# Performance work log

Hardware: AMD Instinct MI355X
Metric: run time of the kernel (lower is better)

Reference implementation:

```python
import jax, jax.numpy as jnp
import numpy as np

EPS = 1e-5  # torch LayerNorm default
DT_RANK = 32  # ceil(d_model=512 / 16)


def layer_norm(x, g, b):
    mu = x.mean(-1, keepdims=True)
    var = x.var(-1, keepdims=True)
    return (x - mu) / jnp.sqrt(var + EPS) * g + b


def conv1d(x, w, b, pad):
    # x: (B, C, L), w: (O, I, K) -- torch Conv1d semantics
    y = jax.lax.conv_general_dilated(x, w, (1,), [(pad, pad)],
                                     dimension_numbers=('NCH', 'OIH', 'NCH'))
    return y + b[None, :, None]


def mamba(u, in_w, conv_w, conv_b, xproj_w, dt_w, dt_b, Alog, D, out_w, d_state, d_conv):
    # Faithful mamba_ssm Mamba block (no biases on in/x/out proj, RMS of official impl)
    Bsz, L, _ = u.shape
    xz = jnp.einsum('bld,ed->ble', u, in_w)          # (B, L, 2*Di)
    x, z = jnp.split(xz, 2, axis=-1)
    Di = x.shape[-1]
    # causal depthwise conv1d, truncated to L (padding=d_conv-1 on the left)
    xc = jax.lax.conv_general_dilated(x.transpose(0, 2, 1), conv_w[:, None, :], (1,),
                                      [(d_conv - 1, 0)],
                                      dimension_numbers=('NCH', 'OIH', 'NCH'),
                                      feature_group_count=Di)
    x = jax.nn.silu((xc + conv_b[None, :, None]).transpose(0, 2, 1))  # (B, L, Di)
    xdb = jnp.einsum('bld,ed->ble', x, xproj_w)       # (B, L, dt_rank + 2*N)
    dt = jax.nn.softplus(jnp.einsum('blr,dr->bld', xdb[..., :DT_RANK], dt_w) + dt_b)
    Bm = xdb[..., DT_RANK:DT_RANK + d_state]          # (B, L, N)
    Cm = xdb[..., DT_RANK + d_state:]                 # (B, L, N)
    A = -jnp.exp(Alog)                                # (Di, N)

    def step(h, ins):
        dt_t, x_t, B_t, C_t = ins                     # (B,Di),(B,Di),(B,N),(B,N)
        dA = jnp.exp(dt_t[..., None] * A)             # (B, Di, N)
        h = dA * h + (dt_t * x_t)[..., None] * B_t[:, None, :]
        y = (h * C_t[:, None, :]).sum(-1)             # (B, Di)
        return h, y

    h0 = jnp.zeros((Bsz, Di, d_state), u.dtype)
    xs = (dt.transpose(1, 0, 2), x.transpose(1, 0, 2),
          Bm.transpose(1, 0, 2), Cm.transpose(1, 0, 2))
    _, ys = jax.lax.scan(step, h0, xs)
    y = ys.transpose(1, 0, 2) + x * D                 # skip via D
    y = y * jax.nn.silu(z)
    return jnp.einsum('bld,od->blo', y, out_w)


def _forward(x, fe_w, fe_b, fe_ln_g, fe_ln_b, emb_ln_g, emb_ln_b,
             conv1_w, conv1_b, conv2_w, conv2_b,
             mf_in_w, mf_conv_w, mf_conv_b, mf_xproj_w, mf_dt_w, mf_dt_b, mf_Alog, mf_D, mf_out_w,
             mb_in_w, mb_conv_w, mb_conv_b, mb_xproj_w, mb_dt_w, mb_dt_b, mb_Alog, mb_D, mb_out_w,
             norm_g, norm_b, fc1_w, fc1_b, fc2_w, fc2_b):
    x = x.reshape(x.shape[0], 100, 23)
    # FrequencyEmbedding: rfft over a length-1 last dim == the signal itself; |.| then Linear+LN+ReLU
    id_mag = jnp.abs(x[..., :1])                      # (B, 100, 1)
    e = jax.nn.relu(layer_norm(id_mag @ fe_w.T + fe_b, fe_ln_g, fe_ln_b))
    id_embed = jax.nn.relu(layer_norm(e, emb_ln_g, emb_ln_b))  # outer LN+ReLU
    data = x[..., 1:].transpose(0, 2, 1)              # (B, 22, 100)
    f1 = jax.nn.relu(conv1d(data, conv1_w, conv1_b, 1))
    f2 = jax.nn.relu(conv1d(f1, conv2_w, conv2_b, 1)).transpose(0, 2, 1)  # (B,100,256)
    comb = jnp.concatenate([id_embed, f2], axis=-1)   # (B, 100, 512)
    fo = mamba(comb, mf_in_w, mf_conv_w, mf_conv_b, mf_xproj_w, mf_dt_w, mf_dt_b,
               mf_Alog, mf_D, mf_out_w, 16, 4)
    bo = mamba(comb[:, ::-1], mb_in_w, mb_conv_w, mb_conv_b, mb_xproj_w, mb_dt_w, mb_dt_b,
               mb_Alog, mb_D, mb_out_w, 8, 2)[:, ::-1]
    pooled = (fo + bo).max(axis=1)                    # (B, 512)
    pooled = layer_norm(pooled, norm_g, norm_b)       # self.norm (undefined in source; LN(512))
    h = jax.nn.relu(pooled @ fc1_w.T + fc1_b)
    return h @ fc2_w.T + fc2_b                        # (B, 4)


def setup_inputs() -> dict:
    key = jax.random.key(0)
    ks = iter(jax.random.split(key, 48))
    def n(shape, s=0.02):
        return jax.random.normal(next(ks), shape, jnp.float32) * s
    Di = 1024
    alog16 = jnp.log(jnp.tile(jnp.arange(1, 17, dtype=jnp.float32), (Di, 1)))
    alog8 = jnp.log(jnp.tile(jnp.arange(1, 9, dtype=jnp.float32), (Di, 1)))
    return {
        'x': jax.random.normal(next(ks), (512, 2300), jnp.float32),
        'fe_w': n((256, 1), 1.0), 'fe_b': jnp.zeros(256, jnp.float32),
        'fe_ln_g': jnp.ones(256, jnp.float32), 'fe_ln_b': jnp.zeros(256, jnp.float32),
        'emb_ln_g': jnp.ones(256, jnp.float32), 'emb_ln_b': jnp.zeros(256, jnp.float32),
        'conv1_w': n((128, 22, 3)), 'conv1_b': jnp.zeros(128, jnp.float32),
        'conv2_w': n((256, 128, 3)), 'conv2_b': jnp.zeros(256, jnp.float32),
        'mf_in_w': n((2 * Di, 512)), 'mf_conv_w': n((Di, 4)), 'mf_conv_b': jnp.zeros(Di, jnp.float32),
        'mf_xproj_w': n((32 + 2 * 16, Di)), 'mf_dt_w': n((Di, 32)), 'mf_dt_b': n((Di,), 0.1),
        'mf_Alog': alog16, 'mf_D': jnp.ones(Di, jnp.float32), 'mf_out_w': n((512, Di)),
        'mb_in_w': n((2 * Di, 512)), 'mb_conv_w': n((Di, 2)), 'mb_conv_b': jnp.zeros(Di, jnp.float32),
        'mb_xproj_w': n((32 + 2 * 8, Di)), 'mb_dt_w': n((Di, 32)), 'mb_dt_b': n((Di,), 0.1),
        'mb_Alog': alog8, 'mb_D': jnp.ones(Di, jnp.float32), 'mb_out_w': n((512, Di)),
        'norm_g': jnp.ones(512, jnp.float32), 'norm_b': jnp.zeros(512, jnp.float32),
        'fc1_w': n((128, 512)), 'fc1_b': jnp.zeros(128, jnp.float32),
        'fc2_w': n((4, 128)), 'fc2_b': jnp.zeros(4, jnp.float32),
    }


def reference(x, fe_w, fe_b, fe_ln_g, fe_ln_b, emb_ln_g, emb_ln_b,
              conv1_w, conv1_b, conv2_w, conv2_b,
              mf_in_w, mf_conv_w, mf_conv_b, mf_xproj_w, mf_dt_w, mf_dt_b, mf_Alog, mf_D, mf_out_w,
              mb_in_w, mb_conv_w, mb_conv_b, mb_xproj_w, mb_dt_w, mb_dt_b, mb_Alog, mb_D, mb_out_w,
              norm_g, norm_b, fc1_w, fc1_b, fc2_w, fc2_b):
    return _forward(x, fe_w, fe_b, fe_ln_g, fe_ln_b, emb_ln_g, emb_ln_b,
                    conv1_w, conv1_b, conv2_w, conv2_b,
                    mf_in_w, mf_conv_w, mf_conv_b, mf_xproj_w, mf_dt_w, mf_dt_b, mf_Alog, mf_D, mf_out_w,
                    mb_in_w, mb_conv_w, mb_conv_b, mb_xproj_w, mb_dt_w, mb_dt_b, mb_Alog, mb_D, mb_out_w,
                    norm_g, norm_b, fc1_w, fc1_b, fc2_w, fc2_b)
```

## Files before the change

### kernel.cpp

```cpp
#include <hip/hip_runtime.h>
#include <cstddef>
#include <cstdint>

#define BSZ 512
#define SEQ 100

typedef __bf16 bf16_t;
typedef __attribute__((ext_vector_type(8))) __bf16 bf16x8;
typedef __attribute__((ext_vector_type(4))) float f32x4;

__device__ __forceinline__ float sigmoidf_(float v){ return 1.f/(1.f + __expf(-v)); }
__device__ __forceinline__ float siluf_(float v){ return v * sigmoidf_(v); }
__device__ __forceinline__ float softplusf_(float v){ return (v > 20.f) ? v : __logf(1.f + __expf(v)); }

__global__ __launch_bounds__(256) void cvt_bf16_kernel(
    const float* __restrict__ src, bf16_t* __restrict__ dst, int n)
{
    int i = blockIdx.x*256 + threadIdx.x;
    if (i < n) dst[i] = (bf16_t)src[i];
}

__global__ __launch_bounds__(256) void prep_outw_kernel(
    const float* __restrict__ of, const float* __restrict__ ob, bf16_t* __restrict__ W)
{
    int i = blockIdx.x*256 + threadIdx.x;
    if (i < 512*2048){
        int o = i >> 11, k = i & 2047;
        W[i] = (bf16_t)((k < 1024) ? of[o*1024 + k] : ob[o*1024 + (k - 1024)]);
    }
}

__global__ __launch_bounds__(256) void prep_convw_kernel(
    const float* __restrict__ c1w, const float* __restrict__ c2w,
    bf16_t* __restrict__ W1p, bf16_t* __restrict__ W2p)
{
    int i = blockIdx.x*256 + threadIdx.x;
    if (i < 128*96){
        int o = i / 96, kk = i - o*96, k = kk >> 5, c = kk & 31;
        W1p[i] = (c < 22) ? (bf16_t)c1w[(o*22 + c)*3 + k] : (bf16_t)0.f;
    }
    if (i < 256*384){
        int o = i / 384, kk = i - o*384, k = kk >> 7, c = kk & 127;
        W2p[i] = (bf16_t)c2w[(o*128 + c)*3 + k];
    }
}

__global__ __launch_bounds__(256) void fe0_kernel(
    const float* __restrict__ x,
    const float* __restrict__ fe_w, const float* __restrict__ fe_b,
    const float* __restrict__ g1, const float* __restrict__ b1,
    const float* __restrict__ g2, const float* __restrict__ b2,
    bf16_t* __restrict__ comb, bf16_t* __restrict__ F0pad, bf16_t* __restrict__ F1pad)
{
    const int b = blockIdx.x;
    const int t = threadIdx.x;
    const int wv = t >> 6, lane = t & 63;

    float few[4], feb[4], lg1[4], lb1[4], lg2[4], lb2[4];
    #pragma unroll
    for (int q = 0; q < 4; ++q){
        int j = lane + 64*q;
        few[q] = fe_w[j]; feb[q] = fe_b[j];
        lg1[q] = g1[j];  lb1[q] = b1[j];
        lg2[q] = g2[j];  lb2[q] = b2[j];
    }
    for (int l = wv; l < SEQ; l += 4){
        float m = fabsf(x[(size_t)(b*SEQ + l)*23]);
        float e[4];
        float s1 = 0.f, s2 = 0.f;
        #pragma unroll
        for (int q = 0; q < 4; ++q){ e[q] = m*few[q] + feb[q]; s1 += e[q]; s2 += e[q]*e[q]; }
        #pragma unroll
        for (int off = 32; off > 0; off >>= 1){ s1 += __shfl_xor(s1, off); s2 += __shfl_xor(s2, off); }
        float mean = s1 * (1.f/256.f);
        float rstd = rsqrtf(s2*(1.f/256.f) - mean*mean + 1e-5f);
        s1 = 0.f; s2 = 0.f;
        #pragma unroll
        for (int q = 0; q < 4; ++q){
            e[q] = fmaxf((e[q]-mean)*rstd*lg1[q] + lb1[q], 0.f);
            s1 += e[q]; s2 += e[q]*e[q];
        }
        #pragma unroll
        for (int off = 32; off > 0; off >>= 1){ s1 += __shfl_xor(s1, off); s2 += __shfl_xor(s2, off); }
        mean = s1 * (1.f/256.f);
        rstd = rsqrtf(s2*(1.f/256.f) - mean*mean + 1e-5f);
        #pragma unroll
        for (int q = 0; q < 4; ++q){
            float v = fmaxf((e[q]-mean)*rstd*lg2[q] + lb2[q], 0.f);
            comb[(size_t)(b*SEQ + l)*512 + lane + 64*q] = (bf16_t)v;
        }
    }

    for (int idx = t; idx < 102*32; idx += 256){
        int r = idx >> 5, c = idx & 31;
        float v = 0.f;
        if (r >= 1 && r <= SEQ && c < 22) v = x[(size_t)(b*SEQ + r - 1)*23 + 1 + c];
        F0pad[(size_t)(b*102 + r)*32 + c] = (bf16_t)v;
    }
    if (t < 128) F1pad[(size_t)(b*102 + 0)*128 + t] = (bf16_t)0.f;
    else F1pad[(size_t)(b*102 + 101)*128 + (t - 128)] = (bf16_t)0.f;
}

__global__ __launch_bounds__(256) void gemm_conv_kernel(
    const bf16_t* __restrict__ Abase, int lda, int Az,
    const bf16_t* __restrict__ W, int K, int N,
    const float* __restrict__ bias,
    bf16_t* __restrict__ Cbase, int ldc, int Cb, int coff, int noff, int Mtot)
{
    __shared__ bf16_t As[128*32];
    __shared__ bf16_t Ws[128*32];
    const bf16_t* A = Abase + (size_t)blockIdx.z * Az;
    const int t = threadIdx.x;
    const int lane = t & 63, w = t >> 6;
    const int n0 = blockIdx.y * 128;
    const int rsub = lane >> 2, csub = lane & 3;
    const int col = lane & 15, quad = lane >> 4;
    const int wOffM = (w & 1) * 64, wOffN = (w >> 1) * 64;

    f32x4 acc[4][4];
    #pragma unroll
    for (int i = 0; i < 4; ++i)
        #pragma unroll
        for (int j = 0; j < 4; ++j)
            acc[i][j] = (f32x4){0.f, 0.f, 0.f, 0.f};

    for (int k0 = 0; k0 < K; k0 += 32){
        __syncthreads();
        #pragma unroll
        for (int q = 0; q < 2; ++q){
            const int rt = w*32 + q*16 + rsub;
            const int lq = csub ^ ((rt >> 1) & 3);
            int ra = (rt < Mtot) ? rt : (Mtot - 1);
            const bf16_t* ga = A + (size_t)ra*lda + k0 + lq*8;
            __builtin_amdgcn_global_load_lds(
                (const __attribute__((address_space(1))) void*)ga,
                (__attribute__((address_space(3))) void*)&As[(w*32 + q*16)*32], 16, 0, 0);
            const bf16_t* gw = W + (size_t)(n0 + rt)*K + k0 + lq*8;
            __builtin_amdgcn_global_load_lds(
                (const __attribute__((address_space(1))) void*)gw,
                (__attribute__((address_space(3))) void*)&Ws[(w*32 + q*16)*32], 16, 0, 0);
        }
        __syncthreads();

        bf16x8 af[4], bfv[4];
        #pragma unroll
        for (int i = 0; i < 4; ++i){
            const int ra = wOffM + i*16 + col;
            af[i]  = *(const bf16x8*)&As[ra*32 + (quad ^ ((ra >> 1) & 3))*8];
            const int rb = wOffN + i*16 + col;
            bfv[i] = *(const bf16x8*)&Ws[rb*32 + (quad ^ ((rb >> 1) & 3))*8];
        }
        #pragma unroll
        for (int i = 0; i < 4; ++i)
            #pragma unroll
            for (int j = 0; j < 4; ++j)
                acc[i][j] = __builtin_amdgcn_mfma_f32_16x16x32_bf16(af[i], bfv[j], acc[i][j], 0, 0, 0);
    }

    #pragma unroll
    for (int i = 0; i < 4; ++i){
        const int gmb = wOffM + i*16 + quad*4;
        #pragma unroll
        for (int j = 0; j < 4; ++j){
            const int gn = n0 + wOffN + j*16 + col;
            const float bb = bias[gn];
            #pragma unroll
            for (int r = 0; r < 4; ++r){
                const int gm = gmb + r;
                if (gm < Mtot){
                    float v = fmaxf(acc[i][j][r] + bb, 0.f);
                    Cbase[((size_t)blockIdx.z*Cb + coff + gm)*ldc + noff + gn] = (bf16_t)v;
                }
            }
        }
    }
}

__global__ __launch_bounds__(256) void gemm_in_kernel(
    const bf16_t* __restrict__ A, int lda, int Mtot,
    const bf16_t* __restrict__ W, int K,
    bf16_t* __restrict__ xy, bf16_t* __restrict__ z)
{
    __shared__ bf16_t smem[128*132];
    bf16_t* As0 = smem;
    bf16_t* As1 = smem + 4096;
    bf16_t* Ws0 = smem + 8192;
    bf16_t* Ws1 = smem + 12288;
    const int t = threadIdx.x;
    const int lane = t & 63, w = t >> 6;
    const int m0 = blockIdx.x * 128, n0 = blockIdx.y * 128;
    const int rsub = lane >> 2, csub = lane & 3;
    const int col = lane & 15, quad = lane >> 4;
    const int wOffM = (w & 1) * 64, wOffN = (w >> 1) * 64;

    f32x4 acc[4][4];
    #pragma unroll
    for (int i = 0; i < 4; ++i)
        #pragma unroll
        for (int j = 0; j < 4; ++j)
            acc[i][j] = (f32x4){0.f, 0.f, 0.f, 0.f};

    for (int k0 = 0; k0 < K; k0 += 64){
        __syncthreads();
        #pragma unroll
        for (int hh = 0; hh < 2; ++hh){
            bf16_t* Asb = hh ? As1 : As0;
            bf16_t* Wsb = hh ? Ws1 : Ws0;
            #pragma unroll
            for (int q = 0; q < 2; ++q){
                const int rt = w*32 + q*16 + rsub;
                const int lq = csub ^ ((rt >> 1) & 3);
                int ra = m0 + rt; ra = (ra < Mtot) ? ra : (Mtot - 1);
                const bf16_t* ga = A + (size_t)ra*lda + k0 + hh*32 + lq*8;
                __builtin_amdgcn_global_load_lds(
                    (const __attribute__((address_space(1))) void*)ga,
                    (__attribute__((address_space(3))) void*)&Asb[(w*32 + q*16)*32], 16, 0, 0);
                const bf16_t* gw = W + (size_t)(n0 + rt)*K + k0 + hh*32 + lq*8;
                __builtin_amdgcn_global_load_lds(
                    (const __attribute__((address_space(1))) void*)gw,
                    (__attribute__((address_space(3))) void*)&Wsb[(w*32 + q*16)*32], 16, 0, 0);
            }
        }
        __syncthreads();

        #pragma unroll
        for (int hh = 0; hh < 2; ++hh){
            bf16_t* Asb = hh ? As1 : As0;
            bf16_t* Wsb = hh ? Ws1 : Ws0;
            bf16x8 af[4], bfv[4];
            #pragma unroll
            for (int i = 0; i < 4; ++i){
                const int ra = wOffM + i*16 + col;
                af[i]  = *(const bf16x8*)&Asb[ra*32 + (quad ^ ((ra >> 1) & 3))*8];
                const int rb = wOffN + i*16 + col;
                bfv[i] = *(const bf16x8*)&Wsb[rb*32 + (quad ^ ((rb >> 1) & 3))*8];
            }
            #pragma unroll
            for (int i = 0; i < 4; ++i)
                #pragma unroll
                for (int j = 0; j < 4; ++j)
                    acc[i][j] = __builtin_amdgcn_mfma_f32_16x16x32_bf16(af[i], bfv[j], acc[i][j], 0, 0, 0);
        }
    }

    __syncthreads();
    #pragma unroll
    for (int i = 0; i < 4; ++i){
        const int row0 = wOffM + i*16 + quad*4;
        #pragma unroll
        for (int j = 0; j < 4; ++j){
            const int cT = wOffN + j*16 + col;
            #pragma unroll
            for (int r = 0; r < 4; ++r)
                smem[(row0 + r)*132 + cT] = (bf16_t)acc[i][j][r];
        }
    }
    __syncthreads();

    const int half = n0 >> 11, within = n0 & 2047;
    bf16_t* dstBase = ((within < 1024) ? xy : z) + half*1024 + (within & 1023);
    #pragma unroll
    for (int k = 0; k < 8; ++k){
        const int idx = t + k*256;
        const int row = idx >> 4;
        const int ch  = (idx & 15) * 8;
        const int gm = m0 + row;
        if (gm < Mtot)
            *(bf16x8*)&dstBase[(size_t)gm*2048 + ch] = *(const bf16x8*)&smem[row*132 + ch];
    }
}

__global__ __launch_bounds__(256) void gemm_out_kernel(
    const bf16_t* __restrict__ A, int Mtot,
    const bf16_t* __restrict__ W,
    float* __restrict__ C)
{
    __shared__ bf16_t As[2][128*32];
    __shared__ bf16_t Ws[2][128*32];
    const int t = threadIdx.x;
    const int lane = t & 63, w = t >> 6;
    const int m0 = blockIdx.x * 128, n0 = blockIdx.y * 128;
    const int rsub = lane >> 2, csub = lane & 3;
    const int col = lane & 15, quad = lane >> 4;
    const int wOffM = (w & 1) * 64, wOffN = (w >> 1) * 64;
    const int K = 2048;

    f32x4 acc[4][4];
    #pragma unroll
    for (int i = 0; i < 4; ++i)
        #pragma unroll
        for (int j = 0; j < 4; ++j)
            acc[i][j] = (f32x4){0.f, 0.f, 0.f, 0.f};

    for (int k0 = 0; k0 < K; k0 += 64){
        __syncthreads();
        #pragma unroll
        for (int hh = 0; hh < 2; ++hh){
            #pragma unroll
            for (int q = 0; q < 2; ++q){
                const int rt = w*32 + q*16 + rsub;
                const int lq = csub ^ ((rt >> 1) & 3);
                int ra = m0 + rt; ra = (ra < Mtot) ? ra : (Mtot - 1);
                const bf16_t* ga = A + (size_t)ra*K + k0 + hh*32 + lq*8;
                __builtin_amdgcn_global_load_lds(
                    (const __attribute__((address_space(1))) void*)ga,
                    (__attribute__((address_space(3))) void*)&As[hh][(w*32 + q*16)*32], 16, 0, 0);
                const bf16_t* gw = W + (size_t)(n0 + rt)*K + k0 + hh*32 + lq*8;
                __builtin_amdgcn_global_load_lds(
                    (const __attribute__((address_space(1))) void*)gw,
                    (__attribute__((address_space(3))) void*)&Ws[hh][(w*32 + q*16)*32], 16, 0, 0);
            }
        }
        __syncthreads();

        #pragma unroll
        for (int hh = 0; hh < 2; ++hh){
            bf16x8 af[4], bfv[4];
            #pragma unroll
            for (int i = 0; i < 4; ++i){
                const int ra = wOffM + i*16 + col;
                af[i]  = *(const bf16x8*)&As[hh][ra*32 + (quad ^ ((ra >> 1) & 3))*8];
                const int rb = wOffN + i*16 + col;
                bfv[i] = *(const bf16x8*)&Ws[hh][rb*32 + (quad ^ ((rb >> 1) & 3))*8];
            }
            #pragma unroll
            for (int i = 0; i < 4; ++i)
                #pragma unroll
                for (int j = 0; j < 4; ++j)
                    acc[i][j] = __builtin_amdgcn_mfma_f32_16x16x32_bf16(af[i], bfv[j], acc[i][j], 0, 0, 0);
        }
    }

    #pragma unroll
    for (int i = 0; i < 4; ++i){
        const int gmb = m0 + wOffM + i*16 + quad*4;
        #pragma unroll
        for (int j = 0; j < 4; ++j){
            const int gn = n0 + wOffN + j*16 + col;
            #pragma unroll
            for (int r = 0; r < 4; ++r){
                const int gm = gmb + r;
                if (gm < Mtot)
                    C[(size_t)gm*512 + gn] = acc[i][j][r];
            }
        }
    }
}

__global__ __launch_bounds__(256) void gemm_x_kernel(
    const bf16_t* __restrict__ xy,
    const bf16_t* __restrict__ Wf, const bf16_t* __restrict__ Wb,
    float* __restrict__ C)
{
    __shared__ bf16_t As[128*32];
    __shared__ bf16_t Ws[64*32];
    const int half = blockIdx.y;
    const bf16_t* A = xy + half*1024;
    const bf16_t* W = half ? Wb : Wf;
    const int N = half ? 48 : 64;
    const int t = threadIdx.x;
    const int lane = t & 63, w = t >> 6;
    const int m0 = blockIdx.x * 128;
    const int rsub = lane >> 2, csub = lane & 3;
    const int col = lane & 15, quad = lane >> 4;

    f32x4 acc[2][4];
    #pragma unroll
    for (int i = 0; i < 2; ++i)
        #pragma unroll
        for (int j = 0; j < 4; ++j)
            acc[i][j] = (f32x4){0.f, 0.f, 0.f, 0.f};

    for (int k0 = 0; k0 < 1024; k0 += 32){
        __syncthreads();
        #pragma unroll
        for (int q = 0; q < 2; ++q){
            const int rt = q*64 + w*16 + rsub;
            const int lq = csub ^ ((rt >> 1) & 3);
            const bf16_t* ga = A + (size_t)(m0 + rt)*2048 + k0 + lq*8;
            __builtin_amdgcn_global_load_lds(
                (const __attribute__((address_space(1))) void*)ga,
                (__attribute__((address_space(3))) void*)&As[(q*64 + w*16)*32], 16, 0, 0);
        }
        {
            const int rt = w*16 + rsub;
            const int lq = csub ^ ((rt >> 1) & 3);
            int rw = (rt < N) ? rt : (N - 1);
            const bf16_t* gw = W + (size_t)rw*1024 + k0 + lq*8;
            __builtin_amdgcn_global_load_lds(
                (const __attribute__((address_space(1))) void*)gw,
                (__attribute__((address_space(3))) void*)&Ws[(w*16)*32], 16, 0, 0);
        }
        __syncthreads();

        bf16x8 af[2], bfv[4];
        #pragma unroll
        for (int i = 0; i < 2; ++i){
            const int ra = w*32 + i*16 + col;
            af[i]  = *(const bf16x8*)&As[ra*32 + (quad ^ ((ra >> 1) & 3))*8];
        }
        #pragma unroll
        for (int j = 0; j < 4; ++j){
            const int rb = j*16 + col;
            bfv[j] = *(const bf16x8*)&Ws[rb*32 + (quad ^ ((rb >> 1) & 3))*8];
        }
        #pragma unroll
        for (int i = 0; i < 2; ++i)
            #pragma unroll
            for (int j = 0; j < 4; ++j)
                acc[i][j] = __builtin_amdgcn_mfma_f32_16x16x32_bf16(af[i], bfv[j], acc[i][j], 0, 0, 0);
    }

    #pragma unroll
    for (int i = 0; i < 2; ++i){
        const int gmb = m0 + w*32 + i*16 + quad*4;
        #pragma unroll
        for (int j = 0; j < 4; ++j){
            const int gn = j*16 + col;
            if (gn < N){
                #pragma unroll
                for (int r = 0; r < 4; ++r)
                    C[(size_t)(gmb + r)*128 + half*64 + gn] = acc[i][j][r];
            }
        }
    }
}

__global__ __launch_bounds__(256) void dt_kernel(
    const float* __restrict__ xdb,
    const float* __restrict__ dtwf, const float* __restrict__ dtbf,
    const float* __restrict__ dtwb, const float* __restrict__ dtbb,
    bf16_t* __restrict__ dtb)
{
    const int half = blockIdx.y >> 3;
    const int d = (blockIdx.y & 7)*128 + (threadIdx.x & 127);
    const int mslot = threadIdx.x >> 7;
    const int m0 = blockIdx.x * 16;
    __shared__ float sd[16*32];
    for (int i = threadIdx.x; i < 16*32; i += 256){
        int r = i >> 5, c = i & 31;
        sd[i] = xdb[(size_t)(m0 + r)*128 + half*64 + c];
    }
    const float* dw = half ? dtwb : dtwf;
    float w[32];
    #pragma unroll
    for (int r = 0; r < 32; ++r) w[r] = dw[d*32 + r];
    const float db = half ? dtbb[d] : dtbf[d];
    __syncthreads();
    #pragma unroll
    for (int i = 0; i < 8; ++i){
        const int row = mslot + i*2;
        const float* rp = &sd[row*32];
        float a = db;
        #pragma unroll
        for (int r = 0; r < 32; ++r) a += w[r]*rp[r];
        dtb[(size_t)(m0 + row)*2048 + half*1024 + d] = (bf16_t)softplusf_(a);
    }
}

template<int DC, bool REV>
__device__ __forceinline__ void conv_dev(bf16_t* base, const float* wsrc, float bias)
{
    float w[DC];
    #pragma unroll
    for (int k = 0; k < DC; ++k) w[k] = wsrc[k];
    float hist[DC-1];
    #pragma unroll
    for (int k = 0; k < DC-1; ++k) hist[k] = 0.f;
    const int step = REV ? -1 : 1;
    int l = REV ? (SEQ-1) : 0;
    for (int t0 = 0; t0 < SEQ; t0 += 10){
        float v[10];
        #pragma unroll
        for (int i = 0; i < 10; ++i) v[i] = (float)base[(size_t)(l + step*i)*2048];
        float o[10];
        #pragma unroll
        for (int i = 0; i < 10; ++i){
            float a = bias + w[DC-1]*v[i];
            #pragma unroll
            for (int j = 1; j < DC; ++j) a += w[DC-1-j]*hist[j-1];
            #pragma unroll
            for (int j = DC-2; j >= 1; --j) hist[j] = hist[j-1];
            hist[0] = v[i];
            o[i] = siluf_(a);
        }
        #pragma unroll
        for (int i = 0; i < 10; ++i)
            base[(size_t)(l + step*i)*2048] = (bf16_t)o[i];
        l += step*10;
    }
}

__global__ __launch_bounds__(256) void conv_silu_kernel(
    bf16_t* __restrict__ xy,
    const float* __restrict__ cwf, const float* __restrict__ cbf,
    const float* __restrict__ cwb, const float* __restrict__ cbb)
{
    const int gid = blockIdx.x*256 + threadIdx.x;
    const int b = gid >> 11, d2 = gid & 2047;
    const int half = d2 >> 10, d = d2 & 1023;
    bf16_t* base = xy + (size_t)b*SEQ*2048 + d2;
    if (half == 0) conv_dev<4, false>(base, cwf + d*4, cbf[d]);
    else           conv_dev<2, true >(base, cwb + d*2, cbb[d]);
}

template<int DS, bool REV, bool STRUCT>
__device__ __forceinline__ void scan_core(
    bf16_t* __restrict__ xybase, const bf16_t* __restrict__ zbase,
    const bf16_t* __restrict__ tbase, const float* __restrict__ sx,
    const float* __restrict__ Av, float Dd)
{
    float h[DS];
    #pragma unroll
    for (int s = 0; s < DS; ++s) h[s] = 0.f;
    const int step = REV ? -1 : 1;
    const float A0 = Av[0];
    int l = REV ? (SEQ-1) : 0;

    for (int t0 = 0; t0 < SEQ; t0 += 10){
        float xr[10], zr[10], tr[10];
        #pragma unroll
        for (int i = 0; i < 10; ++i){
            const size_t li = (size_t)(l + step*i);
            xr[i] = (float)xybase[li*2048];
            zr[i] = (float)zbase[li*2048];
            tr[i] = (float)tbase[li*2048];
        }
        #pragma unroll
        for (int i = 0; i < 10; ++i){
            const int li = l + step*i;
            const float4* sxl4 = (const float4*)&sx[li*2*DS];
            const float dtv = tr[i];
            const float dtx = dtv * xr[i];
            float yv = 0.f;
            if (STRUCT){
                const float r = __expf(dtv*A0);
                float rp = r;
                #pragma unroll
                for (int s4 = 0; s4 < DS/4; ++s4){
                    float4 Bv = sxl4[s4];
                    float4 Cv = sxl4[DS/4 + s4];
                    h[s4*4+0] = rp*h[s4*4+0] + dtx*Bv.x; yv += h[s4*4+0]*Cv.x; rp *= r;
                    h[s4*4+1] = rp*h[s4*4+1] + dtx*Bv.y; yv += h[s4*4+1]*Cv.y; rp *= r;
                    h[s4*4+2] = rp*h[s4*4+2] + dtx*Bv.z; yv += h[s4*4+2]*Cv.z; rp *= r;
                    h[s4*4+3] = rp*h[s4*4+3] + dtx*Bv.w; yv += h[s4*4+3]*Cv.w; rp *= r;
                }
            } else {
                #pragma unroll
                for (int s4 = 0; s4 < DS/4; ++s4){
                    float4 Bv = sxl4[s4];
                    float4 Cv = sxl4[DS/4 + s4];
                    h[s4*4+0] = __expf(dtv*Av[s4*4+0])*h[s4*4+0] + dtx*Bv.x; yv += h[s4*4+0]*Cv.x;
                    h[s4*4+1] = __expf(dtv*Av[s4*4+1])*h[s4*4+1] + dtx*Bv.y; yv += h[s4*4+1]*Cv.y;
                    h[s4*4+2] = __expf(dtv*Av[s4*4+2])*h[s4*4+2] + dtx*Bv.z; yv += h[s4*4+2]*Cv.z;
                    h[s4*4+3] = __expf(dtv*Av[s4*4+3])*h[s4*4+3] + dtx*Bv.w; yv += h[s4*4+3]*Cv.w;
                }
            }
            yv += xr[i]*Dd;
            yv *= siluf_(zr[i]);
            xybase[(size_t)li*2048] = (bf16_t)yv;
        }
        l += step*10;
    }
}

template<int DS, bool REV>
__device__ __forceinline__ void scan_dev(
    bf16_t* __restrict__ xybase, const bf16_t* __restrict__ zbase,
    const bf16_t* __restrict__ tbase, const float* __restrict__ sx,
    const float* __restrict__ Arow, float Dd)
{
    float Av[DS];
    #pragma unroll
    for (int s = 0; s < DS; ++s) Av[s] = -__expf(Arow[s]);
    bool structured = true;
    #pragma unroll
    for (int s = 1; s < DS; ++s)
        structured = structured && (fabsf(Av[s] - (float)(s+1)*Av[0]) <= 1e-4f*(float)(s+1));
    if (structured) scan_core<DS, REV, true >(xybase, zbase, tbase, sx, Av, Dd);
    else            scan_core<DS, REV, false>(xybase, zbase, tbase, sx, Av, Dd);
}

__global__ __launch_bounds__(256) void scan_kernel(
    bf16_t* __restrict__ xy, const bf16_t* __restrict__ z,
    const bf16_t* __restrict__ dtb, const float* __restrict__ xdb,
    const float* __restrict__ Alogf, const float* __restrict__ Dpf,
    const float* __restrict__ Alogb, const float* __restrict__ Dpb)
{
    const int b = blockIdx.x >> 3, s8 = blockIdx.x & 7;
    const int t = threadIdx.x;
    __shared__ float sxF[SEQ*32];
    __shared__ float sxB[SEQ*16];
    const float4* src = (const float4*)(xdb + (size_t)b*SEQ*128);

    {
        float4* dstF = (float4*)sxF;
        for (int i = t; i < SEQ*8; i += 256){
            int row = i >> 3, c = i & 7;
            dstF[row*8 + c] = src[row*32 + 8 + c];
        }
        float4* dstB = (float4*)sxB;
        for (int i = t; i < SEQ*4; i += 256){
            int row = i >> 2, c = i & 3;
            dstB[row*4 + c] = src[row*32 + 24 + c];
        }
    }
    __syncthreads();

    if (t < 128){
        const int d = s8*128 + t;
        const size_t off = (size_t)b*SEQ*2048 + d;
        scan_dev<16, false>(xy + off, z + off, dtb + off, sxF, Alogf + d*16, Dpf[d]);
    } else {
        const int d = s8*128 + (t - 128);
        const size_t off = (size_t)b*SEQ*2048 + 1024 + d;
        scan_dev<8, true>(xy + off, z + off, dtb + off, sxB, Alogb + d*8, Dpb[d]);
    }
}

__global__ __launch_bounds__(256) void head_kernel(
    const float* __restrict__ acc,
    const float* __restrict__ ng, const float* __restrict__ nb,
    const float* __restrict__ w1, const float* __restrict__ b1,
    const float* __restrict__ w2, const float* __restrict__ b2,
    float* __restrict__ out)
{
    const int b = blockIdx.x, t = threadIdx.x;
    __shared__ float4 sm4[256];
    __shared__ float sp[512];
    __shared__ float sh2[256];
    __shared__ float sh[128];
    __shared__ float red1[4], red2[4];
    const float* base = acc + (size_t)b*SEQ*512;

    {
        const int c4 = t & 127, lh = t >> 7;
        float4 m = make_float4(-3.4e38f, -3.4e38f, -3.4e38f, -3.4e38f);
        for (int l = lh*50; l < lh*50 + 50; ++l){
            float4 v = ((const float4*)(base + (size_t)l*512))[c4];
            m.x = fmaxf(m.x, v.x); m.y = fmaxf(m.y, v.y);
            m.z = fmaxf(m.z, v.z); m.w = fmaxf(m.w, v.w);
        }
        sm4[t] = m;
    }
    __syncthreads();
    if (t < 128){
        float4 a = sm4[t], c = sm4[t + 128];
        ((float4*)sp)[t] = make_float4(fmaxf(a.x,c.x), fmaxf(a.y,c.y),
                                       fmaxf(a.z,c.z), fmaxf(a.w,c.w));
    }
    __syncthreads();

    float s1 = 0.f, s2 = 0.f;
    for (int o = t; o < 512; o += 256){ float v = sp[o]; s1 += v; s2 += v*v; }
    #pragma unroll
    for (int off = 32; off > 0; off >>= 1){ s1 += __shfl_xor(s1, off); s2 += __shfl_xor(s2, off); }
    const int wv = t >> 6, lane = t & 63;
    if (lane == 0){ red1[wv] = s1; red2[wv] = s2; }
    __syncthreads();
    if (t == 0){
        float a = 0.f, c = 0.f;
        for (int i = 0; i < 4; ++i){ a += red1[i]; c += red2[i]; }
        float mean = a * (1.f/512.f);
        float var = c * (1.f/512.f) - mean*mean;
        red1[0] = mean; red2[0] = rsqrtf(var + 1e-5f);
    }
    __syncthreads();
    const float mean = red1[0], rstd = red2[0];
    for (int o = t; o < 512; o += 256) sp[o] = (sp[o]-mean)*rstd*ng[o] + nb[o];
    __syncthreads();

    {
        const int o = t & 127, half = t >> 7;
        const float4* wrow = (const float4*)(w1 + (size_t)o*512 + half*256);
        const float4* sp4 = (const float4*)sp + half*64;
        float s = 0.f;
        #pragma unroll 8
        for (int j = 0; j < 64; ++j){
            float4 a = sp4[j], wq = wrow[j];
            s += a.x*wq.x + a.y*wq.y + a.z*wq.z + a.w*wq.w;
        }
        sh2[t] = s;
    }
    __syncthreads();
    if (t < 128) sh[t] = fmaxf(sh2[t] + sh2[t + 128] + b1[t], 0.f);
    __syncthreads();
    if (t < 4){
        float a = b2[t];
        for (int j = 0; j < 128; ++j) a += sh[j]*w2[t*128 + j];
        out[b*4 + t] = a;
    }
}

extern "C" void kernel_launch(void* const* d_in, const int* in_sizes, int n_in,
                              void* d_out, int out_size, void* d_ws, size_t ws_size,
                              hipStream_t stream)
{
    (void)in_sizes; (void)n_in; (void)out_size;
    const float* x        = (const float*)d_in[0];
    const float* fe_w     = (const float*)d_in[1];
    const float* fe_b     = (const float*)d_in[2];
    const float* fe_ln_g  = (const float*)d_in[3];
    const float* fe_ln_b  = (const float*)d_in[4];
    const float* emb_ln_g = (const float*)d_in[5];
    const float* emb_ln_b = (const float*)d_in[6];
    const float* conv1_w  = (const float*)d_in[7];
    const float* conv1_b  = (const float*)d_in[8];
    const float* conv2_w  = (const float*)d_in[9];
    const float* conv2_b  = (const float*)d_in[10];
    const float* mf_in_w  = (const float*)d_in[11];
    const float* mf_conv_w= (const float*)d_in[12];
    const float* mf_conv_b= (const float*)d_in[13];
    const float* mf_xproj = (const float*)d_in[14];
    const float* mf_dt_w  = (const float*)d_in[15];
    const float* mf_dt_b  = (const float*)d_in[16];
    const float* mf_Alog  = (const float*)d_in[17];
    const float* mf_D     = (const float*)d_in[18];
    const float* mf_out_w = (const float*)d_in[19];
    const float* mb_in_w  = (const float*)d_in[20];
    const float* mb_conv_w= (const float*)d_in[21];
    const float* mb_conv_b= (const float*)d_in[22];
    const float* mb_xproj = (const float*)d_in[23];
    const float* mb_dt_w  = (const float*)d_in[24];
    const float* mb_dt_b  = (const float*)d_in[25];
    const float* mb_Alog  = (const float*)d_in[26];
    const float* mb_D     = (const float*)d_in[27];
    const float* mb_out_w = (const float*)d_in[28];
    const float* norm_g   = (const float*)d_in[29];
    const float* norm_b   = (const float*)d_in[30];
    const float* fc1_w    = (const float*)d_in[31];
    const float* fc1_b    = (const float*)d_in[32];
    const float* fc2_w    = (const float*)d_in[33];
    const float* fc2_b    = (const float*)d_in[34];
    float* out = (float*)d_out;

    char* p = (char*)d_ws;
    bf16_t* w_in   = (bf16_t*)p; p += (size_t)4096*512*sizeof(bf16_t);
    bf16_t* w_out  = (bf16_t*)p; p += (size_t)512*2048*sizeof(bf16_t);
    bf16_t* w_xpf  = (bf16_t*)p; p += (size_t)64*1024*sizeof(bf16_t);
    bf16_t* w_xpb  = (bf16_t*)p; p += (size_t)48*1024*sizeof(bf16_t);
    bf16_t* W1p    = (bf16_t*)p; p += (size_t)128*96*sizeof(bf16_t);
    bf16_t* W2p    = (bf16_t*)p; p += (size_t)256*384*sizeof(bf16_t);
    bf16_t* comb_all = (bf16_t*)p; p += (size_t)BSZ*SEQ*512*sizeof(bf16_t);
    const size_t fixed_bytes = (size_t)(p - (char*)d_ws);

    const size_t per_b = (size_t)SEQ * (2048*2 + 2048*2 + 2048*2 + 128*4);
    const size_t budget = (ws_size > fixed_bytes) ? (ws_size - fixed_bytes) : 0;
    int Bc = BSZ;
    while (Bc > 64 && (size_t)Bc * per_b > budget) Bc >>= 1;
    const int nch = BSZ / Bc;
    const int M = Bc * SEQ;

    bf16_t* F0pad = (bf16_t*)p;
    bf16_t* F1pad = F0pad + (size_t)BSZ*102*32;
    bf16_t* xy   = (bf16_t*)p;               p += (size_t)M*2048*sizeof(bf16_t);
    bf16_t* z    = (bf16_t*)p;               p += (size_t)M*2048*sizeof(bf16_t);
    bf16_t* dtb  = (bf16_t*)p;               p += (size_t)M*2048*sizeof(bf16_t);
    float*  xdb  = (float*)p;
    float*  accb = (float*)dtb;

    cvt_bf16_kernel<<<(2048*512+255)/256, 256, 0, stream>>>(mf_in_w, w_in, 2048*512);
    cvt_bf16_kernel<<<(2048*512+255)/256, 256, 0, stream>>>(mb_in_w, w_in + (size_t)2048*512, 2048*512);
    prep_outw_kernel<<<(512*2048+255)/256, 256, 0, stream>>>(mf_out_w, mb_out_w, w_out);
    cvt_bf16_kernel<<<(64*1024+255)/256,  256, 0, stream>>>(mf_xproj, w_xpf, 64*1024);
    cvt_bf16_kernel<<<(48*1024+255)/256,  256, 0, stream>>>(mb_xproj, w_xpb, 48*1024);
    prep_convw_kernel<<<(256*384+255)/256, 256, 0, stream>>>(conv1_w, conv2_w, W1p, W2p);

    fe0_kernel<<<BSZ, 256, 0, stream>>>(x, fe_w, fe_b, fe_ln_g, fe_ln_b,
        emb_ln_g, emb_ln_b, comb_all, F0pad, F1pad);
    gemm_conv_kernel<<<dim3(1, 1, BSZ), 256, 0, stream>>>(
        F0pad, 32, 102*32, W1p, 96, 128, conv1_b, F1pad, 128, 102, 1, 0, SEQ);
    gemm_conv_kernel<<<dim3(1, 2, BSZ), 256, 0, stream>>>(
        F1pad, 128, 102*128, W2p, 384, 256, conv2_b, comb_all, 512, 100, 0, 256, SEQ);

    const int gm128 = M / 128;

    for (int c = 0; c < nch; ++c){
        const size_t b0 = (size_t)c * Bc;
        const bf16_t* comb = comb_all + b0*SEQ*512;

        gemm_in_kernel<<<dim3(gm128, 32), 256, 0, stream>>>(comb, 512, M, w_in, 512, xy, z);
        conv_silu_kernel<<<Bc*2048/256, 256, 0, stream>>>(xy, mf_conv_w, mf_conv_b,
                                                          mb_conv_w, mb_conv_b);
        gemm_x_kernel<<<dim3(gm128, 2), 256, 0, stream>>>(xy, w_xpf, w_xpb, xdb);
        dt_kernel<<<dim3(M/16, 16), 256, 0, stream>>>(xdb, mf_dt_w, mf_dt_b,
                                                      mb_dt_w, mb_dt_b, dtb);
        scan_kernel<<<Bc*8, 256, 0, stream>>>(xy, z, dtb, xdb,
                                              mf_Alog, mf_D, mb_Alog, mb_D);
        gemm_out_kernel<<<dim3(gm128, 4), 256, 0, stream>>>(xy, M, w_out, accb);
        head_kernel<<<Bc, 256, 0, stream>>>(accb, norm_g, norm_b, fc1_w, fc1_b,
                                            fc2_w, fc2_b, out + b0*4);
    }
}
```

Before: 1.529 ms.

## Fuse dt projection and softplus into x-projection GEMM epilogue using MFMA

```diff
diff --git a/kernel.cpp b/kernel.cpp
--- a/kernel.cpp
+++ b/kernel.cpp
@@ -350,13 +350,18 @@
 __global__ __launch_bounds__(256) void gemm_x_kernel(
     const bf16_t* __restrict__ xy,
     const bf16_t* __restrict__ Wf, const bf16_t* __restrict__ Wb,
-    float* __restrict__ C)
+    const bf16_t* __restrict__ dWf, const bf16_t* __restrict__ dWb,
+    const float* __restrict__ dbf, const float* __restrict__ dbb,
+    float* __restrict__ C,
+    bf16_t* __restrict__ dtb)
 {
     __shared__ bf16_t As[128*32];
-    __shared__ bf16_t Ws[64*32];
+    __shared__ bf16_t Ws[128*32];
     const int half = blockIdx.y;
     const bf16_t* A = xy + half*1024;
     const bf16_t* W = half ? Wb : Wf;
+    const bf16_t* dW = half ? dWb : dWf;
+    const float* db = half ? dbb : dbf;
     const int N = half ? 48 : 64;
     const int t = threadIdx.x;
     const int lane = t & 63, w = t >> 6;
@@ -424,37 +429,66 @@
             }
         }
     }
-}
-
-__global__ __launch_bounds__(256) void dt_kernel(
-    const float* __restrict__ xdb,
-    const float* __restrict__ dtwf, const float* __restrict__ dtbf,
-    const float* __restrict__ dtwb, const float* __restrict__ dtbb,
-    bf16_t* __restrict__ dtb)
-{
-    const int half = blockIdx.y >> 3;
-    const int d = (blockIdx.y & 7)*128 + (threadIdx.x & 127);
-    const int mslot = threadIdx.x >> 7;
-    const int m0 = blockIdx.x * 16;
-    __shared__ float sd[16*32];
-    for (int i = threadIdx.x; i < 16*32; i += 256){
-        int r = i >> 5, c = i & 31;
-        sd[i] = xdb[(size_t)(m0 + r)*128 + half*64 + c];
-    }
-    const float* dw = half ? dtwb : dtwf;
-    float w[32];
-    #pragma unroll
-    for (int r = 0; r < 32; ++r) w[r] = dw[d*32 + r];
-    const float db = half ? dtbb[d] : dtbf[d];
-    __syncthreads();
-    #pragma unroll
-    for (int i = 0; i < 8; ++i){
-        const int row = mslot + i*2;
-        const float* rp = &sd[row*32];
-        float a = db;
-        #pragma unroll
-        for (int r = 0; r < 32; ++r) a += w[r]*rp[r];
-        dtb[(size_t)(m0 + row)*2048 + half*1024 + d] = (bf16_t)softplusf_(a);
+
+    __syncthreads();
+    #pragma unroll
+    for (int i = 0; i < 2; ++i){
+        const int row0 = w*32 + i*16 + quad*4;
+        #pragma unroll
+        for (int j = 0; j < 2; ++j){
+            const int cc = j*16 + col;
+            #pragma unroll
+            for (int r = 0; r < 4; ++r){
+                const int row = row0 + r;
+                const int pc = (cc >> 3) ^ ((row >> 1) & 3);
+                As[row*32 + pc*8 + (cc & 7)] = (bf16_t)acc[i][j][r];
+            }
+        }
+    }
+
+    const int wOffM = (w & 1)*64, wOffN = (w >> 1)*64;
+    for (int n2 = 0; n2 < 8; ++n2){
+        __syncthreads();
+        #pragma unroll
+        for (int q = 0; q < 2; ++q){
+            const int rt = w*32 + q*16 + rsub;
+            const int lq = csub ^ ((rt >> 1) & 3);
+            const bf16_t* gw = dW + (size_t)(n2*128 + rt)*32 + lq*8;
+            __builtin_amdgcn_global_load_lds(
+                (const __attribute__((address_space(1))) void*)gw,
+                (__attribute__((address_space(3))) void*)&Ws[(w*32 + q*16)*32], 16, 0, 0);
+        }
+        __syncthreads();
+
+        bf16x8 af[4], bfv[4];
+        #pragma unroll
+        for (int i = 0; i < 4; ++i){
+            const int ra = wOffM + i*16 + col;
+            af[i]  = *(const bf16x8*)&As[ra*32 + (quad ^ ((ra >> 1) & 3))*8];
+            const int rb = wOffN + i*16 + col;
+            bfv[i] = *(const bf16x8*)&Ws[rb*32 + (quad ^ ((rb >> 1) & 3))*8];
+        }
+        f32x4 a2[4][4];
+        #pragma unroll
+        for (int i = 0; i < 4; ++i)
+            #pragma unroll
+            for (int j = 0; j < 4; ++j)
+                a2[i][j] = __builtin_amdgcn_mfma_f32_16x16x32_bf16(
+                    af[i], bfv[j], (f32x4){0.f,0.f,0.f,0.f}, 0, 0, 0);
+
+        #pragma unroll
+        for (int i = 0; i < 4; ++i){
+            const int gmb = m0 + wOffM + i*16 + quad*4;
+            #pragma unroll
+            for (int j = 0; j < 4; ++j){
+                const int gn = n2*128 + wOffN + j*16 + col;
+                const float bb = db[gn];
+                #pragma unroll
+                for (int r = 0; r < 4; ++r)
+                    dtb[(size_t)(gmb + r)*2048 + half*1024 + gn] =
+                        (bf16_t)softplusf_(a2[i][j][r] + bb);
+            }
+        }
     }
 }
 
@@ -472,7 +506,7 @@
     for (int t0 = 0; t0 < SEQ; t0 += 10){
         float v[10];
         #pragma unroll
-        for (int i = 0; i < 10; ++i) v[i] = (float)base[(size_t)(l + step*i)*2048];
+        for (int i = 0; i < 10; ++i) v[i] = (float)base[(l + step*i)*2048];
         float o[10];
         #pragma unroll
         for (int i = 0; i < 10; ++i){
@@ -486,7 +520,7 @@
         }
         #pragma unroll
         for (int i = 0; i < 10; ++i)
-            base[(size_t)(l + step*i)*2048] = (bf16_t)o[i];
+            base[(l + step*i)*2048] = (bf16_t)o[i];
         l += step*10;
     }
 }
@@ -521,10 +555,10 @@
         float xr[10], zr[10], tr[10];
         #pragma unroll
         for (int i = 0; i < 10; ++i){
-            const size_t li = (size_t)(l + step*i);
-            xr[i] = (float)xybase[li*2048];
-            zr[i] = (float)zbase[li*2048];
-            tr[i] = (float)tbase[li*2048];
+            const int li = (l + step*i)*2048;
+            xr[i] = (float)xybase[li];
+            zr[i] = (float)zbase[li];
+            tr[i] = (float)tbase[li];
         }
         #pragma unroll
         for (int i = 0; i < 10; ++i){
@@ -558,7 +592,7 @@
             }
             yv += xr[i]*Dd;
             yv *= siluf_(zr[i]);
-            xybase[(size_t)li*2048] = (bf16_t)yv;
+            xybase[li*2048] = (bf16_t)yv;
         }
         l += step*10;
     }
@@ -739,6 +773,8 @@
     bf16_t* w_out  = (bf16_t*)p; p += (size_t)512*2048*sizeof(bf16_t);
     bf16_t* w_xpf  = (bf16_t*)p; p += (size_t)64*1024*sizeof(bf16_t);
     bf16_t* w_xpb  = (bf16_t*)p; p += (size_t)48*1024*sizeof(bf16_t);
+    bf16_t* w_dtf  = (bf16_t*)p; p += (size_t)1024*32*sizeof(bf16_t);
+    bf16_t* w_dtb  = (bf16_t*)p; p += (size_t)1024*32*sizeof(bf16_t);
     bf16_t* W1p    = (bf16_t*)p; p += (size_t)128*96*sizeof(bf16_t);
     bf16_t* W2p    = (bf16_t*)p; p += (size_t)256*384*sizeof(bf16_t);
     bf16_t* comb_all = (bf16_t*)p; p += (size_t)BSZ*SEQ*512*sizeof(bf16_t);
@@ -764,6 +800,8 @@
     prep_outw_kernel<<<(512*2048+255)/256, 256, 0, stream>>>(mf_out_w, mb_out_w, w_out);
     cvt_bf16_kernel<<<(64*1024+255)/256,  256, 0, stream>>>(mf_xproj, w_xpf, 64*1024);
     cvt_bf16_kernel<<<(48*1024+255)/256,  256, 0, stream>>>(mb_xproj, w_xpb, 48*1024);
+    cvt_bf16_kernel<<<(1024*32+255)/256,  256, 0, stream>>>(mf_dt_w, w_dtf, 1024*32);
+    cvt_bf16_kernel<<<(1024*32+255)/256,  256, 0, stream>>>(mb_dt_w, w_dtb, 1024*32);
     prep_convw_kernel<<<(256*384+255)/256, 256, 0, stream>>>(conv1_w, conv2_w, W1p, W2p);
 
     fe0_kernel<<<BSZ, 256, 0, stream>>>(x, fe_w, fe_b, fe_ln_g, fe_ln_b,
@@ -782,9 +820,9 @@
         gemm_in_kernel<<<dim3(gm128, 32), 256, 0, stream>>>(comb, 512, M, w_in, 512, xy, z);
         conv_silu_kernel<<<Bc*2048/256, 256, 0, stream>>>(xy, mf_conv_w, mf_conv_b,
                                                           mb_conv_w, mb_conv_b);
-        gemm_x_kernel<<<dim3(gm128, 2), 256, 0, stream>>>(xy, w_xpf, w_xpb, xdb);
-        dt_kernel<<<dim3(M/16, 16), 256, 0, stream>>>(xdb, mf_dt_w, mf_dt_b,
-                                                      mb_dt_w, mb_dt_b, dtb);
+        gemm_x_kernel<<<dim3(gm128, 2), 256, 0, stream>>>(xy, w_xpf, w_xpb,
+                                                          w_dtf, w_dtb, mf_dt_b, mb_dt_b,
+                                                          xdb, dtb);
         scan_kernel<<<Bc*8, 256, 0, stream>>>(xy, z, dtb, xdb,
                                               mf_Alog, mf_D, mb_Alog, mb_D);
         gemm_out_kernel<<<dim3(gm128, 4), 256, 0, stream>>>(xy, M, w_out, accb);
```

Measured after the change: 1.651 ms. 1.08x slower.
